# Kernel tuning notes

Measured on AMD Instinct MI355X. Metric: run time of the kernel, lower is better.

The kernel has to match this reference:

```python
import jax, jax.numpy as jnp
import numpy as np

B, T, D_MODEL, N_HEADS = 2, 2048, 1024, 16


def setup_inputs() -> dict:
    key = jax.random.key(0)
    ks = jax.random.split(key, 5)
    w_scale = 0.02
    return {
        "x": jax.random.normal(ks[0], (B, T, D_MODEL), jnp.float32),
        "Wq": jax.random.normal(ks[1], (D_MODEL, D_MODEL), jnp.float32) * w_scale,
        "Wk": jax.random.normal(ks[2], (D_MODEL, D_MODEL), jnp.float32) * w_scale,
        "Wv": jax.random.normal(ks[3], (D_MODEL, D_MODEL), jnp.float32) * w_scale,
        "Wo": jax.random.normal(ks[4], (D_MODEL, D_MODEL), jnp.float32) * w_scale,
    }


def reference(x, Wq, Wk, Wv, Wo):
    Bv, Tv, _ = x.shape
    H = N_HEADS
    D = D_MODEL // H
    # Projections (torch nn.Linear: y = x @ W.T), split heads -> (B, H, T, D)
    q = (x @ Wq.T).reshape(Bv, Tv, H, D).transpose(0, 2, 1, 3)
    k = (x @ Wk.T).reshape(Bv, Tv, H, D).transpose(0, 2, 1, 3)
    v = (x @ Wv.T).reshape(Bv, Tv, H, D).transpose(0, 2, 1, 3)

    scale = jnp.sqrt(jnp.asarray(D, jnp.float32))
    scores = jnp.einsum("bhqd,bhkd->bhqk", q, k) / scale  # (B, H, T, T)

    # ALiBi bias: -|i-j| * slope_h, future positions masked to -inf (causal)
    slopes = jnp.asarray(
        [2.0 ** (-8.0 * h / H) for h in range(1, H + 1)], jnp.float32
    )
    pos = jnp.arange(Tv)
    dist = jnp.abs(pos[None, :] - pos[:, None]).astype(jnp.float32)  # (T, T)
    bias = -dist[None, :, :] * slopes[:, None, None]                 # (H, T, T)
    causal_mask = jnp.triu(jnp.ones((Tv, Tv), dtype=bool), 1)
    bias = jnp.where(causal_mask[None, :, :], -jnp.inf, bias)
    scores = scores + bias[None]  # (B, H, T, T)

    attn = jax.nn.softmax(scores, axis=-1)
    out = jnp.einsum("bhqk,bhkd->bhqd", attn, v)
    out = out.transpose(0, 2, 1, 3).reshape(Bv, Tv, D_MODEL)
    return out @ Wo.T
```

## Files before the change

### kernel.cpp

```cpp
#include <hip/hip_runtime.h>


#define DEV __device__ __forceinline__

typedef __attribute__((ext_vector_type(8))) short short8;
typedef __attribute__((ext_vector_type(4))) float f32x4;
typedef __attribute__((ext_vector_type(16))) float f32x16;
typedef __attribute__((ext_vector_type(4))) unsigned short ushort4v;
typedef __attribute__((ext_vector_type(4))) unsigned uint4v;

DEV unsigned short f2bf(float f) {
  unsigned u = __builtin_bit_cast(unsigned, f);
  u += 0x7fffu + ((u >> 16) & 1u);
  return (unsigned short)(u >> 16);
}
DEV float bf2f(unsigned short u) {
  unsigned x = ((unsigned)u) << 16;
  return __builtin_bit_cast(float, x);
}
DEV unsigned cvtpk_bf(float lo, float hi) {
  unsigned r;
  asm("v_cvt_pk_bf16_f32 %0, %1, %2" : "=v"(r) : "v"(lo), "v"(hi));
  return r;
}

DEV void gl2lds16(const void* g, void* l) {
  __builtin_amdgcn_global_load_lds(
      (const __attribute__((address_space(1))) void*)g,
      (__attribute__((address_space(3))) void*)l, 16, 0, 0);
}

__global__ __launch_bounds__(256) void cvt_all(
    const float* __restrict__ x, const float* __restrict__ wq,
    const float* __restrict__ wk, const float* __restrict__ wv,
    const float* __restrict__ wo, unsigned short* __restrict__ xb,
    unsigned short* __restrict__ wqb, unsigned short* __restrict__ wkb,
    unsigned short* __restrict__ wvb, unsigned short* __restrict__ wob) {
  int b = blockIdx.x;
  const float* s;
  unsigned short* d;
  int off;
  if (b < 4096)      { s = x;  d = xb;  off = b; }
  else if (b < 5120) { s = wq; d = wqb; off = b - 4096; }
  else if (b < 6144) { s = wk; d = wkb; off = b - 5120; }
  else if (b < 7168) { s = wv; d = wvb; off = b - 6144; }
  else               { s = wo; d = wob; off = b - 7168; }
  int i = (off * 256 + threadIdx.x) * 4;
  float4 v = *(const float4*)(s + i);
  ushort4v o = {f2bf(v.x), f2bf(v.y), f2bf(v.z), f2bf(v.w)};
  *(ushort4v*)(d + i) = o;
}

__global__ __launch_bounds__(512, 2) void gemm_qkv(
    const unsigned short* __restrict__ A, const unsigned short* __restrict__ Wq,
    const unsigned short* __restrict__ Wk, const unsigned short* __restrict__ Wv,
    unsigned short* __restrict__ Qo, unsigned short* __restrict__ Ko,
    unsigned short* __restrict__ Vo) {
  constexpr int K = 1024;
  __shared__ alignas(16) unsigned short Sm[65536];
  const int t = threadIdx.x;
  const int w = t >> 6, l = t & 63, l15 = l & 15, l4 = l >> 4;
  const int wr = w >> 2, wc = w & 3;
  const int wsel = blockIdx.x >> 2;
  const int n0 = (blockIdx.x & 3) * 256;
  const int m0 = blockIdx.y * 256;
  const unsigned short* Bmat = (wsel == 0) ? Wq : ((wsel == 1) ? Wk : Wv);

  const int srow = t >> 3;
  const int sk = ((t & 7) ^ (srow & 7)) * 8;

#define STG_A(T, H)                                                           \
  {                                                                           \
    gl2lds16(A + (m0 + (H)*128 + srow) * K + (T)*64 + sk,                     \
             &Sm[((T)&1) * 16384 + (H)*8192 + t * 8]);                        \
    gl2lds16(A + (m0 + (H)*128 + 64 + srow) * K + (T)*64 + sk,                \
             &Sm[((T)&1) * 16384 + (H)*8192 + 4096 + t * 8]);                 \
  }
#define STG_B(T, H)                                                           \
  {                                                                           \
    gl2lds16(Bmat + (n0 + (H)*128 + srow) * K + (T)*64 + sk,                  \
             &Sm[32768 + ((T)&1) * 16384 + (H)*8192 + t * 8]);                \
    gl2lds16(Bmat + (n0 + (H)*128 + 64 + srow) * K + (T)*64 + sk,             \
             &Sm[32768 + ((T)&1) * 16384 + (H)*8192 + 4096 + t * 8]);         \
  }

  f32x4 acc[8][4];
  {
    f32x4 z4 = {0.f, 0.f, 0.f, 0.f};
#pragma unroll
    for (int i = 0; i < 8; i++)
#pragma unroll
      for (int j = 0; j < 4; j++) acc[i][j] = z4;
  }
  short8 af[4][2], bf[2][2][2];

#define RD_AF(TT, QM)                                                         \
  {                                                                           \
    const unsigned short* Ab_ = &Sm[((TT)&1) * 16384];                        \
    _Pragma("unroll") for (int mi_ = 0; mi_ < 4; mi_++) {                     \
      _Pragma("unroll") for (int kk_ = 0; kk_ < 2; kk_++) {                   \
        af[mi_][kk_] = *(const short8*)&Ab_[                                  \
            (wr * 128 + (QM)*64 + mi_ * 16 + l15) * 64 +                      \
            (((kk_ * 4 + l4) ^ (l15 & 7)) * 8)];                              \
      }                                                                       \
    }                                                                         \
  }
#define RD_BF(TT, QN)                                                         \
  {                                                                           \
    const unsigned short* Bb_ = &Sm[32768 + ((TT)&1) * 16384];                \
    _Pragma("unroll") for (int ni_ = 0; ni_ < 2; ni_++) {                     \
      _Pragma("unroll") for (int kk_ = 0; kk_ < 2; kk_++) {                   \
        bf[(QN)][ni_][kk_] = *(const short8*)&Bb_[                            \
            (wc * 64 + (QN)*32 + ni_ * 16 + l15) * 64 +                       \
            (((kk_ * 4 + l4) ^ (l15 & 7)) * 8)];                              \
      }                                                                       \
    }                                                                         \
  }
#define DO_MFMA(QM, QN)                                                       \
  {                                                                           \
    _Pragma("unroll") for (int mi_ = 0; mi_ < 4; mi_++) {                     \
      _Pragma("unroll") for (int ni_ = 0; ni_ < 2; ni_++) {                   \
        _Pragma("unroll") for (int kk_ = 0; kk_ < 2; kk_++) {                 \
          acc[(QM)*4 + mi_][(QN)*2 + ni_] =                                   \
              __builtin_amdgcn_mfma_f32_16x16x32_bf16(                        \
                  af[mi_][kk_], bf[(QN)][ni_][kk_],                           \
                  acc[(QM)*4 + mi_][(QN)*2 + ni_], 0, 0, 0);                  \
        }                                                                     \
      }                                                                       \
    }                                                                         \
  }

#define VMW4 asm volatile("s_waitcnt vmcnt(4)" ::: "memory")
#define VMW0 asm volatile("s_waitcnt vmcnt(0)" ::: "memory")
#define NOW ((void)0)
#define PHASE(RDS, STG, MFMA_, WAIT)                                          \
  {                                                                           \
    RDS;                                                                      \
    STG;                                                                      \
    __builtin_amdgcn_s_barrier();                                             \
    __builtin_amdgcn_s_setprio(1);                                            \
    MFMA_;                                                                    \
    __builtin_amdgcn_s_setprio(0);                                            \
    WAIT;                                                                     \
    __builtin_amdgcn_s_barrier();                                             \
  }

  STG_B(0, 0); STG_B(0, 1); STG_A(0, 0); STG_A(0, 1);
  STG_B(1, 0); STG_B(1, 1);
  VMW4;
  __builtin_amdgcn_s_barrier();

#pragma unroll 1
  for (int i = 0; i < 7; ++i) {
    const int TA = 2 * i, TB = TA + 1;
    PHASE(RD_AF(TA, 0); RD_BF(TA, 0), STG_A(TB, 0),     DO_MFMA(0, 0), NOW);
    PHASE(RD_BF(TA, 1),               STG_A(TB, 1),     DO_MFMA(0, 1), NOW);
    PHASE(RD_AF(TA, 1),               STG_B(TA + 2, 0), DO_MFMA(1, 0), NOW);
    PHASE(NOW,                        STG_B(TA + 2, 1), DO_MFMA(1, 1), VMW4);
    PHASE(RD_AF(TB, 0); RD_BF(TB, 0), STG_A(TA + 2, 0), DO_MFMA(0, 0), NOW);
    PHASE(RD_BF(TB, 1),               STG_A(TA + 2, 1), DO_MFMA(0, 1), NOW);
    PHASE(RD_AF(TB, 1),               STG_B(TB + 2, 0), DO_MFMA(1, 0), NOW);
    PHASE(NOW,                        STG_B(TB + 2, 1), DO_MFMA(1, 1), VMW4);
  }
  PHASE(RD_AF(14, 0); RD_BF(14, 0), STG_A(15, 0), DO_MFMA(0, 0), NOW);
  PHASE(RD_BF(14, 1),               STG_A(15, 1), DO_MFMA(0, 1), NOW);
  PHASE(RD_AF(14, 1),               NOW,          DO_MFMA(1, 0), NOW);
  PHASE(NOW,                        NOW,          DO_MFMA(1, 1), VMW0);
  PHASE(RD_AF(15, 0); RD_BF(15, 0), NOW,          DO_MFMA(0, 0), NOW);
  PHASE(RD_BF(15, 1),               NOW,          DO_MFMA(0, 1), NOW);
  PHASE(RD_AF(15, 1),               NOW,          DO_MFMA(1, 0), NOW);
  PHASE(NOW,                        NOW,          DO_MFMA(1, 1), NOW);

#undef PHASE
#undef NOW
#undef VMW0
#undef VMW4
#undef DO_MFMA
#undef RD_BF
#undef RD_AF
#undef STG_B
#undef STG_A

  if (wsel != 2) {
    unsigned short* D = (wsel == 0) ? Qo : Ko;
    const float scale = (wsel == 0) ? 0.18033688011112042f : 1.0f;
    const int zb = (n0 >> 6) + wc;
#pragma unroll
    for (int mi = 0; mi < 8; mi++)
#pragma unroll
      for (int r = 0; r < 4; r++) {
        int m = m0 + wr * 128 + mi * 16 + l4 * 4 + r;
        int b = m >> 11, tt = m & 2047;
        int z = b * 16 + zb;
#pragma unroll
        for (int ni = 0; ni < 4; ni++)
          D[(z * 2048 + tt) * 64 + ni * 16 + l15] = f2bf(acc[mi][ni][r] * scale);
      }
  } else {
    unsigned short* Tr = Sm + w * 4608;
    const int b = (m0 + wr * 128) >> 11, tbase = (m0 + wr * 128) & 2047;
    const int zg = b * 16 + (n0 >> 6) + wc;
#pragma unroll
    for (int p = 0; p < 2; p++) {
#pragma unroll
      for (int mi = 0; mi < 4; mi++)
#pragma unroll
        for (int ni = 0; ni < 4; ni++) {
          int mg = p * 4 + mi;
          ushort4v pk = {f2bf(acc[mg][ni][0]), f2bf(acc[mg][ni][1]),
                         f2bf(acc[mg][ni][2]), f2bf(acc[mg][ni][3])};
          *(ushort4v*)&Tr[(ni * 16 + l15) * 72 + mi * 16 + l4 * 4] = pk;
        }
      asm volatile("s_waitcnt lgkmcnt(0)" ::: "memory");
      __builtin_amdgcn_sched_barrier(0);
#pragma unroll
      for (int j = 0; j < 8; j++) {
        int idx = j * 64 + l;
        int d = idx >> 3, c = idx & 7;
        int t0 = (c >> 1) * 16 + (c & 1) * 4;
        ushort4v lo4 = *(const ushort4v*)&Tr[d * 72 + t0];
        ushort4v hi4 = *(const ushort4v*)&Tr[d * 72 + t0 + 8];
        short8 v = {(short)lo4[0], (short)lo4[1], (short)lo4[2], (short)lo4[3],
                    (short)hi4[0], (short)hi4[1], (short)hi4[2], (short)hi4[3]};
        *(short8*)&Vo[(zg * 64 + d) * 2048 + tbase + p * 64 + c * 8] = v;
      }
      asm volatile("s_waitcnt lgkmcnt(0)" ::: "memory");
      __builtin_amdgcn_sched_barrier(0);
    }
  }
}

__global__ __launch_bounds__(256, 2) void gemm_o(
    const unsigned short* __restrict__ A, const unsigned short* __restrict__ Bm,
    float* __restrict__ C) {
  constexpr int K = 1024;
  __shared__ alignas(16) unsigned short Al[128 * 32];
  __shared__ alignas(16) unsigned short Bl[64 * 32];
  const int t = threadIdx.x;
  const int l = t & 63, l15 = l & 15, l4 = l >> 4;
  const int wm = ((t >> 6) & 1) * 64, wn = (t >> 7) * 32;
  const int sblk = (blockIdx.x & 7) * 64 + (blockIdx.x >> 3);
  const int m0 = (sblk >> 4) * 128, n0 = (sblk & 15) * 64;

  f32x4 zero4 = {0.f, 0.f, 0.f, 0.f};
  f32x4 acc[4][2];
#pragma unroll
  for (int i = 0; i < 4; i++)
#pragma unroll
    for (int j = 0; j < 2; j++) acc[i][j] = zero4;

  const int row0 = t >> 2, seg = (t & 3) * 8;
  const unsigned short* Ag0 = A + (m0 + row0) * K + seg;
  const unsigned short* Ag1 = A + (m0 + row0 + 64) * K + seg;
  const unsigned short* Bg0 = Bm + (n0 + row0) * K + seg;

  for (int k0 = 0; k0 < K; k0 += 32) {
    gl2lds16(Ag0 + k0, &Al[t * 8]);
    gl2lds16(Ag1 + k0, &Al[2048 + t * 8]);
    gl2lds16(Bg0 + k0, &Bl[t * 8]);
    __syncthreads();
    short8 af[4], bf2[2];
#pragma unroll
    for (int mi = 0; mi < 4; mi++)
      af[mi] = *(const short8*)&Al[(wm + mi * 16 + l15) * 32 + l4 * 8];
#pragma unroll
    for (int ni = 0; ni < 2; ni++)
      bf2[ni] = *(const short8*)&Bl[(wn + ni * 16 + l15) * 32 + l4 * 8];
#pragma unroll
    for (int mi = 0; mi < 4; mi++)
#pragma unroll
      for (int ni = 0; ni < 2; ni++)
        acc[mi][ni] = __builtin_amdgcn_mfma_f32_16x16x32_bf16(
            af[mi], bf2[ni], acc[mi][ni], 0, 0, 0);
    __syncthreads();
  }
#pragma unroll
  for (int mi = 0; mi < 4; mi++)
#pragma unroll
    for (int r = 0; r < 4; r++) {
      int m = m0 + wm + mi * 16 + l4 * 4 + r;
      float* cp = C + m * 1024 + n0 + wn + l15;
      cp[0] = acc[mi][0][r];
      cp[16] = acc[mi][1][r];
    }
}

__global__ __launch_bounds__(256, 3) void flash_alibi(
    const unsigned short* __restrict__ Q, const unsigned short* __restrict__ Kb,
    const unsigned short* __restrict__ Vt, unsigned short* __restrict__ O0,
    unsigned short* __restrict__ O1, float* __restrict__ L0,
    float* __restrict__ L1) {
  __shared__ alignas(16) unsigned short Kl[2 * 4096];
  __shared__ alignas(16) unsigned short Vl[2 * 4096];
  const int t = threadIdx.x, w = t >> 6, l = t & 63;
  const int l31 = l & 31, h = l >> 5, lsw = l31 & 7;
  const int g = blockIdx.x;
  const int qt = 15 - (g >> 6);
  const int z = (g & 63) >> 1, s = g & 1;
  const int q0 = qt * 128, hd = z & 15;
  const float slope2 = exp2f(-0.5f * (float)(hd + 1)) * 1.4426950408889634f;
  const int qrow = q0 + w * 32;
  const int qi = qrow + l31;

  short8 qf[4];
#pragma unroll
  for (int ks = 0; ks < 4; ks++)
    qf[ks] = *(const short8*)&Q[(z * 2048 + qi) * 64 + ks * 16 + h * 8];

  f32x16 binit;
#pragma unroll
  for (int r = 0; r < 16; r++)
    binit[r] =
        fmaf(slope2, (float)((r & 3) + 8 * (r >> 2) + 4 * h - qi), -10.0f);

  f32x16 accO[2];
  float lsum = 0.f;
#pragma unroll
  for (int nd = 0; nd < 2; nd++)
#pragma unroll
    for (int r = 0; r < 16; r++) accO[nd][r] = 0.f;

  const int sr = t >> 3, sgr = t & 7;
  const int it0 = s ? (qt + 1) : 0;
  const int nt = qt + 1;

#define ISSUE_LOADS(KV0, BUF)                                                 \
  {                                                                           \
    unsigned short* Kd = &Kl[(BUF) * 4096];                                   \
    unsigned short* Vd = &Vl[(BUF) * 4096];                                   \
    const int sx = (sgr ^ (sr & 7)) * 8;                                      \
    gl2lds16(&Kb[(z * 2048 + (KV0) + sr) * 64 + sx], &Kd[t * 8]);             \
    gl2lds16(&Kb[(z * 2048 + (KV0) + 32 + sr) * 64 + sx],                     \
             &Kd[2048 + t * 8]);                                              \
    gl2lds16(&Vt[(z * 64 + sr) * 2048 + (KV0) + sx], &Vd[t * 8]);             \
    gl2lds16(&Vt[(z * 64 + 32 + sr) * 2048 + (KV0) + sx],                     \
             &Vd[2048 + t * 8]);                                              \
  }

  ISSUE_LOADS(it0 * 64, 0)

  for (int ii = 0; ii < nt; ++ii) {
    __syncthreads();
    const int kv0 = (it0 + ii) * 64;
    if (ii + 1 < nt) ISSUE_LOADS(kv0 + 64, (ii + 1) & 1)
    if (kv0 > qrow + 31) continue;
    const unsigned short* Kc = &Kl[(ii & 1) * 4096];
    const unsigned short* Vc = &Vl[(ii & 1) * 4096];

    f32x16 accS[2];
    accS[0] = binit;
    accS[1] = binit;
#pragma unroll
    for (int ks = 0; ks < 4; ks++) {
      short8 kf0 =
          *(const short8*)&Kc[l31 * 64 + (((ks * 2 + h) ^ lsw) * 8)];
      short8 kf1 =
          *(const short8*)&Kc[(32 + l31) * 64 + (((ks * 2 + h) ^ lsw) * 8)];
      accS[0] = __builtin_amdgcn_mfma_f32_32x32x16_bf16(kf0, qf[ks], accS[0],
                                                        0, 0, 0);
      accS[1] = __builtin_amdgcn_mfma_f32_32x32x16_bf16(kf1, qf[ks], accS[1],
                                                        0, 0, 0);
    }

    const bool needMask = (kv0 + 63 > qrow);
#pragma unroll
    for (int ni = 0; ni < 2; ni++) {
      const float fkv = (float)(kv0 + 32 * ni);
      float ps[16];
#pragma unroll
      for (int r = 0; r < 16; r++)
        ps[r] = __builtin_amdgcn_exp2f(fmaf(slope2, fkv, accS[ni][r]));
      if (needMask) {
        const int kb = kv0 + 32 * ni + 4 * h;
#pragma unroll
        for (int r = 0; r < 16; r++)
          if (kb + ((r & 3) + 8 * (r >> 2)) > qi) ps[r] = 0.f;
      }
      lsum += (((ps[0] + ps[1]) + (ps[2] + ps[3])) +
               ((ps[4] + ps[5]) + (ps[6] + ps[7]))) +
              (((ps[8] + ps[9]) + (ps[10] + ps[11])) +
               ((ps[12] + ps[13]) + (ps[14] + ps[15])));
      unsigned pk[8];
#pragma unroll
      for (int i = 0; i < 8; i++) pk[i] = cvtpk_bf(ps[2 * i], ps[2 * i + 1]);
#pragma unroll
      for (int kp = 0; kp < 2; kp++) {
        uint4v pw = {pk[kp * 4 + 0], pk[kp * 4 + 1], pk[kp * 4 + 2],
                     pk[kp * 4 + 3]};
        short8 pa = __builtin_bit_cast(short8, pw);
#pragma unroll
        for (int nd = 0; nd < 2; nd++) {
          short8 vf = *(const short8*)&Vc[(nd * 32 + l31) * 64 +
                                          ((((ni * 2 + kp) * 2 + h) ^ lsw) * 8)];
          accO[nd] = __builtin_amdgcn_mfma_f32_32x32x16_bf16(pa, vf, accO[nd],
                                                             0, 0, 0);
        }
      }
    }
  }
#undef ISSUE_LOADS

  unsigned short* Op = s ? O1 : O0;
  float* Lp = s ? L1 : L0;
  float lv = lsum + __shfl_xor(lsum, 32);
  if (l < 32) Lp[z * 2048 + qrow + l] = lv;
#pragma unroll
  for (int nd = 0; nd < 2; nd++)
#pragma unroll
    for (int r = 0; r < 16; r++) {
      int tg = qrow + (r & 3) + 8 * (r >> 2) + 4 * h;
      Op[(z * 2048 + tg) * 64 + nd * 32 + l31] = f2bf(accO[nd][r]);
    }
}

__global__ __launch_bounds__(256) void combine(
    const unsigned short* __restrict__ O0, const unsigned short* __restrict__ O1,
    const float* __restrict__ L0, const float* __restrict__ L1,
    unsigned short* __restrict__ Ob) {
  int idx = (blockIdx.x * 256 + threadIdx.x) * 8;
  int z = idx >> 17, rem = idx & 131071;
  int tt = rem >> 6, d = rem & 63;
  short8 a = *(const short8*)(O0 + idx);
  short8 b = *(const short8*)(O1 + idx);
  float inv = 1.0f / (L0[z * 2048 + tt] + L1[z * 2048 + tt]);
  short8 o;
#pragma unroll
  for (int j = 0; j < 8; j++) {
    float v = (bf2f((unsigned short)a[j]) + bf2f((unsigned short)b[j])) * inv;
    o[j] = (short)f2bf(v);
  }
  int bq = z >> 4, h = z & 15;
  *(short8*)(Ob + (bq * 2048 + tt) * 1024 + h * 64 + d) = o;
}

extern "C" void kernel_launch(void* const* d_in, const int* in_sizes, int n_in,
                              void* d_out, int out_size, void* d_ws,
                              size_t ws_size, hipStream_t stream) {
  const float* x = (const float*)d_in[0];
  const float* Wq = (const float*)d_in[1];
  const float* Wk = (const float*)d_in[2];
  const float* Wv = (const float*)d_in[3];
  const float* Wo = (const float*)d_in[4];

  char* p = (char*)d_ws;
  unsigned short* xb = (unsigned short*)p;  p += 4096 * 1024 * 2;
  unsigned short* wqb = (unsigned short*)p; p += 1024 * 1024 * 2;
  unsigned short* wkb = (unsigned short*)p; p += 1024 * 1024 * 2;
  unsigned short* wvb = (unsigned short*)p; p += 1024 * 1024 * 2;
  unsigned short* wob = (unsigned short*)p; p += 1024 * 1024 * 2;
  unsigned short* Qb = (unsigned short*)p;  p += 32 * 2048 * 64 * 2;
  unsigned short* Kbf = (unsigned short*)p; p += 32 * 2048 * 64 * 2;
  unsigned short* Vtb = (unsigned short*)p; p += 32 * 2048 * 64 * 2;
  unsigned short* O1 = (unsigned short*)p;  p += 32 * 2048 * 64 * 2;
  float* L0 = (float*)p;                    p += 32 * 2048 * 4;
  float* L1 = (float*)p;                    p += 32 * 2048 * 4;
  unsigned short* O0 = xb;
  unsigned short* Ob = Qb;

  cvt_all<<<8192, 256, 0, stream>>>(x, Wq, Wk, Wv, Wo, xb, wqb, wkb, wvb, wob);
  gemm_qkv<<<dim3(12, 16), 512, 0, stream>>>(xb, wqb, wkb, wvb, Qb, Kbf, Vtb);
  flash_alibi<<<1024, 256, 0, stream>>>(Qb, Kbf, Vtb, O0, O1, L0, L1);
  combine<<<2048, 256, 0, stream>>>(O0, O1, L0, L1, Ob);
  gemm_o<<<512, 256, 0, stream>>>(Ob, wob, (float*)d_out);
}
```

Before: 165.0 us.

## Retile fused QKV GEMM to 256x192 tiles and split out V transpose

The QKV projection now treats the three bf16 weight matrices as one contiguous 3072-row matrix and tiles it 256x192, giving 256 blocks instead of 192. This matches the CU count better and reduces the partially idle last wave. It also swizzles the block order. The in-kernel LDS transpose for V is replaced by plain row-major stores into a new workspace buffer, followed by a separate vtrans kernel. That kernel adds a launch and an extra 8 MB read/write pass over V in exchange for a simpler, uniform epilogue.

Result: no change. 165.3 us (+0.2%).

```diff
diff --git a/kernel.cpp b/kernel.cpp
--- a/kernel.cpp
+++ b/kernel.cpp
@@ -52,19 +52,17 @@
 }
 
 __global__ __launch_bounds__(512, 2) void gemm_qkv(
-    const unsigned short* __restrict__ A, const unsigned short* __restrict__ Wq,
-    const unsigned short* __restrict__ Wk, const unsigned short* __restrict__ Wv,
+    const unsigned short* __restrict__ A, const unsigned short* __restrict__ Ws,
     unsigned short* __restrict__ Qo, unsigned short* __restrict__ Ko,
-    unsigned short* __restrict__ Vo) {
+    unsigned short* __restrict__ Vpl) {
   constexpr int K = 1024;
-  __shared__ alignas(16) unsigned short Sm[65536];
+  __shared__ alignas(16) unsigned short Sm[57344];
   const int t = threadIdx.x;
   const int w = t >> 6, l = t & 63, l15 = l & 15, l4 = l >> 4;
-  const int wr = w >> 2, wc = w & 3;
-  const int wsel = blockIdx.x >> 2;
-  const int n0 = (blockIdx.x & 3) * 256;
-  const int m0 = blockIdx.y * 256;
-  const unsigned short* Bmat = (wsel == 0) ? Wq : ((wsel == 1) ? Wk : Wv);
+  const int wr = w >> 1, wc = w & 1;
+  const int sblk = (blockIdx.x & 7) * 32 + (blockIdx.x >> 3);
+  const int m0 = (sblk >> 4) * 256;
+  const int n0 = (sblk & 15) * 192;
 
   const int srow = t >> 3;
   const int sk = ((t & 7) ^ (srow & 7)) * 8;
@@ -76,61 +74,63 @@
     gl2lds16(A + (m0 + (H)*128 + 64 + srow) * K + (T)*64 + sk,                \
              &Sm[((T)&1) * 16384 + (H)*8192 + 4096 + t * 8]);                 \
   }
-#define STG_B(T, H)                                                           \
-  {                                                                           \
-    gl2lds16(Bmat + (n0 + (H)*128 + srow) * K + (T)*64 + sk,                  \
-             &Sm[32768 + ((T)&1) * 16384 + (H)*8192 + t * 8]);                \
-    gl2lds16(Bmat + (n0 + (H)*128 + 64 + srow) * K + (T)*64 + sk,             \
-             &Sm[32768 + ((T)&1) * 16384 + (H)*8192 + 4096 + t * 8]);         \
-  }
-
-  f32x4 acc[8][4];
+#define STG_B3(T)                                                             \
+  {                                                                           \
+    gl2lds16(Ws + (n0 + srow) * K + (T)*64 + sk,                              \
+             &Sm[32768 + ((T)&1) * 12288 + t * 8]);                           \
+    gl2lds16(Ws + (n0 + 64 + srow) * K + (T)*64 + sk,                         \
+             &Sm[32768 + ((T)&1) * 12288 + 4096 + t * 8]);                    \
+    gl2lds16(Ws + (n0 + 128 + srow) * K + (T)*64 + sk,                        \
+             &Sm[32768 + ((T)&1) * 12288 + 8192 + t * 8]);                    \
+  }
+
+  f32x4 acc[4][6];
   {
     f32x4 z4 = {0.f, 0.f, 0.f, 0.f};
 #pragma unroll
-    for (int i = 0; i < 8; i++)
-#pragma unroll
-      for (int j = 0; j < 4; j++) acc[i][j] = z4;
-  }
-  short8 af[4][2], bf[2][2][2];
+    for (int i = 0; i < 4; i++)
+#pragma unroll
+      for (int j = 0; j < 6; j++) acc[i][j] = z4;
+  }
+  short8 af[2][2], bf[2][3][2];
 
 #define RD_AF(TT, QM)                                                         \
   {                                                                           \
     const unsigned short* Ab_ = &Sm[((TT)&1) * 16384];                        \
-    _Pragma("unroll") for (int mi_ = 0; mi_ < 4; mi_++) {                     \
+    _Pragma("unroll") for (int mi_ = 0; mi_ < 2; mi_++) {                     \
       _Pragma("unroll") for (int kk_ = 0; kk_ < 2; kk_++) {                   \
         af[mi_][kk_] = *(const short8*)&Ab_[                                  \
-            (wr * 128 + (QM)*64 + mi_ * 16 + l15) * 64 +                      \
+            (wr * 64 + (QM)*32 + mi_ * 16 + l15) * 64 +                       \
             (((kk_ * 4 + l4) ^ (l15 & 7)) * 8)];                              \
       }                                                                       \
     }                                                                         \
   }
 #define RD_BF(TT, QN)                                                         \
   {                                                                           \
-    const unsigned short* Bb_ = &Sm[32768 + ((TT)&1) * 16384];                \
-    _Pragma("unroll") for (int ni_ = 0; ni_ < 2; ni_++) {                     \
+    const unsigned short* Bb_ = &Sm[32768 + ((TT)&1) * 12288];                \
+    _Pragma("unroll") for (int ni_ = 0; ni_ < 3; ni_++) {                     \
       _Pragma("unroll") for (int kk_ = 0; kk_ < 2; kk_++) {                   \
         bf[(QN)][ni_][kk_] = *(const short8*)&Bb_[                            \
-            (wc * 64 + (QN)*32 + ni_ * 16 + l15) * 64 +                       \
+            (wc * 96 + (QN)*48 + ni_ * 16 + l15) * 64 +                       \
             (((kk_ * 4 + l4) ^ (l15 & 7)) * 8)];                              \
       }                                                                       \
     }                                                                         \
   }
 #define DO_MFMA(QM, QN)                                                       \
   {                                                                           \
-    _Pragma("unroll") for (int mi_ = 0; mi_ < 4; mi_++) {                     \
-      _Pragma("unroll") for (int ni_ = 0; ni_ < 2; ni_++) {                   \
+    _Pragma("unroll") for (int mi_ = 0; mi_ < 2; mi_++) {                     \
+      _Pragma("unroll") for (int ni_ = 0; ni_ < 3; ni_++) {                   \
         _Pragma("unroll") for (int kk_ = 0; kk_ < 2; kk_++) {                 \
-          acc[(QM)*4 + mi_][(QN)*2 + ni_] =                                   \
+          acc[(QM)*2 + mi_][(QN)*3 + ni_] =                                   \
               __builtin_amdgcn_mfma_f32_16x16x32_bf16(                        \
                   af[mi_][kk_], bf[(QN)][ni_][kk_],                           \
-                  acc[(QM)*4 + mi_][(QN)*2 + ni_], 0, 0, 0);                  \
+                  acc[(QM)*2 + mi_][(QN)*3 + ni_], 0, 0, 0);                  \
         }                                                                     \
       }                                                                       \
     }                                                                         \
   }
 
-#define VMW4 asm volatile("s_waitcnt vmcnt(4)" ::: "memory")
+#define VMW3 asm volatile("s_waitcnt vmcnt(3)" ::: "memory")
 #define VMW0 asm volatile("s_waitcnt vmcnt(0)" ::: "memory")
 #define NOW ((void)0)
 #define PHASE(RDS, STG, MFMA_, WAIT)                                          \
@@ -145,9 +145,9 @@
     __builtin_amdgcn_s_barrier();                                             \
   }
 
-  STG_B(0, 0); STG_B(0, 1); STG_A(0, 0); STG_A(0, 1);
-  STG_B(1, 0); STG_B(1, 1);
-  VMW4;
+  STG_B3(0); STG_A(0, 0); STG_A(0, 1);
+  STG_B3(1);
+  VMW3;
   __builtin_amdgcn_s_barrier();
 
 #pragma unroll 1
@@ -155,12 +155,12 @@
     const int TA = 2 * i, TB = TA + 1;
     PHASE(RD_AF(TA, 0); RD_BF(TA, 0), STG_A(TB, 0),     DO_MFMA(0, 0), NOW);
     PHASE(RD_BF(TA, 1),               STG_A(TB, 1),     DO_MFMA(0, 1), NOW);
-    PHASE(RD_AF(TA, 1),               STG_B(TA + 2, 0), DO_MFMA(1, 0), NOW);
-    PHASE(NOW,                        STG_B(TA + 2, 1), DO_MFMA(1, 1), VMW4);
+    PHASE(RD_AF(TA, 1),               STG_B3(TA + 2),   DO_MFMA(1, 0), NOW);
+    PHASE(NOW,                        NOW,              DO_MFMA(1, 1), VMW3);
     PHASE(RD_AF(TB, 0); RD_BF(TB, 0), STG_A(TA + 2, 0), DO_MFMA(0, 0), NOW);
     PHASE(RD_BF(TB, 1),               STG_A(TA + 2, 1), DO_MFMA(0, 1), NOW);
-    PHASE(RD_AF(TB, 1),               STG_B(TB + 2, 0), DO_MFMA(1, 0), NOW);
-    PHASE(NOW,                        STG_B(TB + 2, 1), DO_MFMA(1, 1), VMW4);
+    PHASE(RD_AF(TB, 1),               STG_B3(TB + 2),   DO_MFMA(1, 0), NOW);
+    PHASE(NOW,                        NOW,              DO_MFMA(1, 1), VMW3);
   }
   PHASE(RD_AF(14, 0); RD_BF(14, 0), STG_A(15, 0), DO_MFMA(0, 0), NOW);
   PHASE(RD_BF(14, 1),               STG_A(15, 1), DO_MFMA(0, 1), NOW);
@@ -174,59 +174,56 @@
 #undef PHASE
 #undef NOW
 #undef VMW0
-#undef VMW4
+#undef VMW3
 #undef DO_MFMA
 #undef RD_BF
 #undef RD_AF
-#undef STG_B
+#undef STG_B3
 #undef STG_A
 
-  if (wsel != 2) {
-    unsigned short* D = (wsel == 0) ? Qo : Ko;
-    const float scale = (wsel == 0) ? 0.18033688011112042f : 1.0f;
-    const int zb = (n0 >> 6) + wc;
-#pragma unroll
-    for (int mi = 0; mi < 8; mi++)
-#pragma unroll
-      for (int r = 0; r < 4; r++) {
-        int m = m0 + wr * 128 + mi * 16 + l4 * 4 + r;
-        int b = m >> 11, tt = m & 2047;
-        int z = b * 16 + zb;
-#pragma unroll
-        for (int ni = 0; ni < 4; ni++)
-          D[(z * 2048 + tt) * 64 + ni * 16 + l15] = f2bf(acc[mi][ni][r] * scale);
+  const float sQ = 0.18033688011112042f;
+#pragma unroll
+  for (int a = 0; a < 4; a++)
+#pragma unroll
+    for (int r = 0; r < 4; r++) {
+      int m = m0 + wr * 64 + a * 16 + l4 * 4 + r;
+      int bq = m >> 11, tt = m & 2047;
+#pragma unroll
+      for (int b = 0; b < 6; b++) {
+        int c16 = n0 + wc * 96 + b * 16;
+        int mat = c16 >> 10, cc = c16 & 1023;
+        unsigned short* D = (mat == 0) ? Qo : ((mat == 1) ? Ko : Vpl);
+        float scale = (mat == 0) ? sQ : 1.0f;
+        int z = bq * 16 + (cc >> 6);
+        D[(z * 2048 + tt) * 64 + (cc & 63) + l15] = f2bf(acc[a][b][r] * scale);
       }
-  } else {
-    unsigned short* Tr = Sm + w * 4608;
-    const int b = (m0 + wr * 128) >> 11, tbase = (m0 + wr * 128) & 2047;
-    const int zg = b * 16 + (n0 >> 6) + wc;
-#pragma unroll
-    for (int p = 0; p < 2; p++) {
-#pragma unroll
-      for (int mi = 0; mi < 4; mi++)
-#pragma unroll
-        for (int ni = 0; ni < 4; ni++) {
-          int mg = p * 4 + mi;
-          ushort4v pk = {f2bf(acc[mg][ni][0]), f2bf(acc[mg][ni][1]),
-                         f2bf(acc[mg][ni][2]), f2bf(acc[mg][ni][3])};
-          *(ushort4v*)&Tr[(ni * 16 + l15) * 72 + mi * 16 + l4 * 4] = pk;
-        }
-      asm volatile("s_waitcnt lgkmcnt(0)" ::: "memory");
-      __builtin_amdgcn_sched_barrier(0);
-#pragma unroll
-      for (int j = 0; j < 8; j++) {
-        int idx = j * 64 + l;
-        int d = idx >> 3, c = idx & 7;
-        int t0 = (c >> 1) * 16 + (c & 1) * 4;
-        ushort4v lo4 = *(const ushort4v*)&Tr[d * 72 + t0];
-        ushort4v hi4 = *(const ushort4v*)&Tr[d * 72 + t0 + 8];
-        short8 v = {(short)lo4[0], (short)lo4[1], (short)lo4[2], (short)lo4[3],
-                    (short)hi4[0], (short)hi4[1], (short)hi4[2], (short)hi4[3]};
-        *(short8*)&Vo[(zg * 64 + d) * 2048 + tbase + p * 64 + c * 8] = v;
-      }
-      asm volatile("s_waitcnt lgkmcnt(0)" ::: "memory");
-      __builtin_amdgcn_sched_barrier(0);
     }
+}
+
+__global__ __launch_bounds__(256) void vtrans(
+    const unsigned short* __restrict__ Vp, unsigned short* __restrict__ Vt) {
+  __shared__ unsigned short Tr[64 * 72];
+  const int t = threadIdx.x;
+  const int z = blockIdx.y, t0 = blockIdx.x * 64;
+#pragma unroll
+  for (int it = 0; it < 2; it++) {
+    int idx = it * 256 + t;
+    int row = idx >> 3, c = idx & 7;
+    short8 v = *(const short8*)&Vp[((z * 2048) + t0 + row) * 64 + c * 8];
+#pragma unroll
+    for (int j = 0; j < 8; j++) Tr[(c * 8 + j) * 72 + row] = (unsigned short)v[j];
+  }
+  __syncthreads();
+#pragma unroll
+  for (int it = 0; it < 2; it++) {
+    int idx = it * 256 + t;
+    int d = idx >> 3, c = idx & 7;
+    int tb = (c >> 1) * 16 + (c & 1) * 4;
+    ushort4v lo4 = *(const ushort4v*)&Tr[d * 72 + tb];
+    ushort4v hi4 = *(const ushort4v*)&Tr[d * 72 + tb + 8];
+    short8 o = {(short)lo4[0], (short)lo4[1], (short)lo4[2], (short)lo4[3],
+                (short)hi4[0], (short)hi4[1], (short)hi4[2], (short)hi4[3]};
+    *(short8*)&Vt[(z * 64 + d) * 2048 + t0 + c * 8] = o;
   }
 }
 
@@ -454,11 +451,13 @@
   unsigned short* O1 = (unsigned short*)p;  p += 32 * 2048 * 64 * 2;
   float* L0 = (float*)p;                    p += 32 * 2048 * 4;
   float* L1 = (float*)p;                    p += 32 * 2048 * 4;
+  unsigned short* Vpl = (unsigned short*)p; p += 32 * 2048 * 64 * 2;
   unsigned short* O0 = xb;
   unsigned short* Ob = Qb;
 
   cvt_all<<<8192, 256, 0, stream>>>(x, Wq, Wk, Wv, Wo, xb, wqb, wkb, wvb, wob);
-  gemm_qkv<<<dim3(12, 16), 512, 0, stream>>>(xb, wqb, wkb, wvb, Qb, Kbf, Vtb);
+  gemm_qkv<<<256, 512, 0, stream>>>(xb, wqb, Qb, Kbf, Vpl);
+  vtrans<<<dim3(32, 32), 256, 0, stream>>>(Vpl, Vtb);
   flash_alibi<<<1024, 256, 0, stream>>>(Qb, Kbf, Vtb, O0, O1, L0, L1);
   combine<<<2048, 256, 0, stream>>>(O0, O1, L0, L1, Ob);
   gemm_o<<<512, 256, 0, stream>>>(Ob, wob, (float*)d_out);
```

## Drop split-KV in flash attention and fuse normalization into epilogue

Applied to the files above, without the earlier changes.

Each attention block now walks the full causal key range for its query tile instead of splitting it into two halves. Normalization by the row sum happens in the kernel epilogue through a small shared-memory table, and the output goes straight to the head-interleaved layout. This removes the separate combine kernel and the partial O/L buffers, saving a launch and a round trip of intermediate data through memory. The cost is half as many blocks and per-block work that doubles for late query tiles, which risks worse load balance and lower occupancy across the CUs.

After: 174.6 us. 5.8% more time.

```diff
diff --git a/kernel.cpp b/kernel.cpp
--- a/kernel.cpp
+++ b/kernel.cpp
@@ -287,16 +287,15 @@
 
 __global__ __launch_bounds__(256, 3) void flash_alibi(
     const unsigned short* __restrict__ Q, const unsigned short* __restrict__ Kb,
-    const unsigned short* __restrict__ Vt, unsigned short* __restrict__ O0,
-    unsigned short* __restrict__ O1, float* __restrict__ L0,
-    float* __restrict__ L1) {
+    const unsigned short* __restrict__ Vt, unsigned short* __restrict__ Ob) {
   __shared__ alignas(16) unsigned short Kl[2 * 4096];
   __shared__ alignas(16) unsigned short Vl[2 * 4096];
+  __shared__ float Lsh[128];
   const int t = threadIdx.x, w = t >> 6, l = t & 63;
   const int l31 = l & 31, h = l >> 5, lsw = l31 & 7;
   const int g = blockIdx.x;
-  const int qt = 15 - (g >> 6);
-  const int z = (g & 63) >> 1, s = g & 1;
+  const int qt = 15 - (g >> 5);
+  const int z = g & 31;
   const int q0 = qt * 128, hd = z & 15;
   const float slope2 = exp2f(-0.5f * (float)(hd + 1)) * 1.4426950408889634f;
   const int qrow = q0 + w * 32;
@@ -321,8 +320,7 @@
     for (int r = 0; r < 16; r++) accO[nd][r] = 0.f;
 
   const int sr = t >> 3, sgr = t & 7;
-  const int it0 = s ? (qt + 1) : 0;
-  const int nt = qt + 1;
+  const int nt = 2 * (qt + 1);
 
 #define ISSUE_LOADS(KV0, BUF)                                                 \
   {                                                                           \
@@ -333,15 +331,15 @@
     gl2lds16(&Kb[(z * 2048 + (KV0) + 32 + sr) * 64 + sx],                     \
              &Kd[2048 + t * 8]);                                              \
     gl2lds16(&Vt[(z * 64 + sr) * 2048 + (KV0) + sx], &Vd[t * 8]);             \
-    gl2lds16(&Vt[(z * 64 + 32 + sr) * 2048 + (KV0) + sx],                     \
+    gl2lds16(&Vt[(z * 64 + 32 + sr) * 2048 + (KV0) + 32 + sx - 32],           \
              &Vd[2048 + t * 8]);                                              \
   }
 
-  ISSUE_LOADS(it0 * 64, 0)
+  ISSUE_LOADS(0, 0)
 
   for (int ii = 0; ii < nt; ++ii) {
     __syncthreads();
-    const int kv0 = (it0 + ii) * 64;
+    const int kv0 = ii * 64;
     if (ii + 1 < nt) ISSUE_LOADS(kv0 + 64, (ii + 1) & 1)
     if (kv0 > qrow + 31) continue;
     const unsigned short* Kc = &Kl[(ii & 1) * 4096];
@@ -400,37 +398,21 @@
   }
 #undef ISSUE_LOADS
 
-  unsigned short* Op = s ? O1 : O0;
-  float* Lp = s ? L1 : L0;
   float lv = lsum + __shfl_xor(lsum, 32);
-  if (l < 32) Lp[z * 2048 + qrow + l] = lv;
+  float inv = 1.0f / lv;
+  if (l < 32) Lsh[w * 32 + l31] = inv;
+  asm volatile("s_waitcnt lgkmcnt(0)" ::: "memory");
+  const int bq = z >> 4, hh = z & 15;
 #pragma unroll
   for (int nd = 0; nd < 2; nd++)
 #pragma unroll
     for (int r = 0; r < 16; r++) {
-      int tg = qrow + (r & 3) + 8 * (r >> 2) + 4 * h;
-      Op[(z * 2048 + tg) * 64 + nd * 32 + l31] = f2bf(accO[nd][r]);
+      int row = (r & 3) + 8 * (r >> 2) + 4 * h;
+      int tg = qrow + row;
+      float iv = Lsh[w * 32 + row];
+      Ob[(bq * 2048 + tg) * 1024 + hh * 64 + nd * 32 + l31] =
+          f2bf(accO[nd][r] * iv);
     }
-}
-
-__global__ __launch_bounds__(256) void combine(
-    const unsigned short* __restrict__ O0, const unsigned short* __restrict__ O1,
-    const float* __restrict__ L0, const float* __restrict__ L1,
-    unsigned short* __restrict__ Ob) {
-  int idx = (blockIdx.x * 256 + threadIdx.x) * 8;
-  int z = idx >> 17, rem = idx & 131071;
-  int tt = rem >> 6, d = rem & 63;
-  short8 a = *(const short8*)(O0 + idx);
-  short8 b = *(const short8*)(O1 + idx);
-  float inv = 1.0f / (L0[z * 2048 + tt] + L1[z * 2048 + tt]);
-  short8 o;
-#pragma unroll
-  for (int j = 0; j < 8; j++) {
-    float v = (bf2f((unsigned short)a[j]) + bf2f((unsigned short)b[j])) * inv;
-    o[j] = (short)f2bf(v);
-  }
-  int bq = z >> 4, h = z & 15;
-  *(short8*)(Ob + (bq * 2048 + tt) * 1024 + h * 64 + d) = o;
 }
 
 extern "C" void kernel_launch(void* const* d_in, const int* in_sizes, int n_in,
@@ -451,15 +433,10 @@
   unsigned short* Qb = (unsigned short*)p;  p += 32 * 2048 * 64 * 2;
   unsigned short* Kbf = (unsigned short*)p; p += 32 * 2048 * 64 * 2;
   unsigned short* Vtb = (unsigned short*)p; p += 32 * 2048 * 64 * 2;
-  unsigned short* O1 = (unsigned short*)p;  p += 32 * 2048 * 64 * 2;
-  float* L0 = (float*)p;                    p += 32 * 2048 * 4;
-  float* L1 = (float*)p;                    p += 32 * 2048 * 4;
-  unsigned short* O0 = xb;
-  unsigned short* Ob = Qb;
+  unsigned short* Ob = (unsigned short*)p;  p += 32 * 2048 * 64 * 2;
 
   cvt_all<<<8192, 256, 0, stream>>>(x, Wq, Wk, Wv, Wo, xb, wqb, wkb, wvb, wob);
   gemm_qkv<<<dim3(12, 16), 512, 0, stream>>>(xb, wqb, wkb, wvb, Qb, Kbf, Vtb);
-  flash_alibi<<<1024, 256, 0, stream>>>(Qb, Kbf, Vtb, O0, O1, L0, L1);
-  combine<<<2048, 256, 0, stream>>>(O0, O1, L0, L1, Ob);
+  flash_alibi<<<512, 256, 0, stream>>>(Qb, Kbf, Vtb, Ob);
   gemm_o<<<512, 256, 0, stream>>>(Ob, wob, (float*)d_out);
 }
```
